# Performance work log

Hardware: AMD Instinct MI355X
Metric: run time of the kernel (lower is better)

Reference implementation:

```python
import jax, jax.numpy as jnp
import numpy as np

B, S, E, H = 4, 2048, 512, 1024

def setup_inputs() -> dict:
    key = jax.random.key(0)
    ks = jax.random.split(key, 8)
    s = 1.0 / np.sqrt(H)
    return {
        "hidden_states": jax.random.normal(ks[0], (B, S, H), jnp.float32),
        "external_embeddings": jax.random.normal(ks[1], (B, E, H), jnp.float32),
        "Wq": jax.random.normal(ks[2], (H, H), jnp.float32) * s,
        "bq": jax.random.normal(ks[3], (H,), jnp.float32) * 0.02,
        "Wk": jax.random.normal(ks[4], (H, H), jnp.float32) * s,
        "bk": jax.random.normal(ks[5], (H,), jnp.float32) * 0.02,
        "Wv": jax.random.normal(ks[6], (H, H), jnp.float32) * s,
        "bv": jax.random.normal(ks[7], (H,), jnp.float32) * 0.02,
    }

def reference(hidden_states, external_embeddings, Wq, bq, Wk, bk, Wv, bv):
    # Projections (torch Linear semantics: here weights stored as [in,out])
    q = hidden_states @ Wq + bq              # [B,S,H]
    k_tok = hidden_states @ Wk + bk          # [B,S,H]
    v_tok = hidden_states @ Wv + bv          # [B,S,H]
    k_ext = external_embeddings @ Wk + bk    # [B,E,H]
    v_ext = external_embeddings @ Wv + bv    # [B,E,H]
    # Each token attends to [its own key] ++ [external keys]; NO 1/sqrt(d) scaling
    # and NO head splitting, matching the original forward exactly.
    s_self = jnp.einsum('bsh,bsh->bs', q, k_tok)[..., None]   # [B,S,1]
    s_ext = jnp.einsum('bsh,beh->bse', q, k_ext)              # [B,S,E]
    scores = jnp.concatenate([s_self, s_ext], axis=-1)        # [B,S,1+E]
    probs = jax.nn.softmax(scores, axis=-1)
    ctx = probs[..., :1] * v_tok + jnp.einsum('bse,beh->bsh', probs[..., 1:], v_ext)
    return ctx  # [B,S,H]
```

## Files before the change

### kernel.cpp

```cpp
#include <hip/hip_runtime.h>
#include <stdint.h>

#define BB 4
#define SS 2048
#define EE 512
#define HH 1024

typedef _Float16 f16;
typedef __attribute__((ext_vector_type(8))) _Float16 f16x8;
typedef __attribute__((ext_vector_type(4))) _Float16 f16x4;
typedef __attribute__((ext_vector_type(4))) float f32x4;

__device__ __forceinline__ void async16(void* lds, const void* g) {
  __builtin_amdgcn_global_load_lds(
      (const __attribute__((address_space(1))) unsigned int*)g,
      (__attribute__((address_space(3))) unsigned int*)lds, 16, 0, 0);
}

#define MFMA16 __builtin_amdgcn_mfma_f32_16x16x32_f16

__global__ __launch_bounds__(256) void prep_kernel(
    const float* __restrict__ xh32, const float* __restrict__ xe32,
    const float* __restrict__ Wq, const float* __restrict__ Wk,
    const float* __restrict__ Wv,
    f16* __restrict__ xh, f16* __restrict__ xe,
    f16* __restrict__ wt_hi, f16* __restrict__ wt_lo) {
  __shared__ float tile[32][33];
  const int bid = blockIdx.x;
  if (bid < 10240) {
    const int i = bid * 256 + threadIdx.x;
    const int n4h = 8192 * HH / 4;
    const float* src = i < n4h ? xh32 : xe32;
    f16* dst = i < n4h ? xh : xe;
    const int k = i < n4h ? i : i - n4h;
    const float4 v = ((const float4*)src)[k];
    f16x4 o;
    o.x = (f16)v.x; o.y = (f16)v.y; o.z = (f16)v.z; o.w = (f16)v.w;
    ((f16x4*)dst)[k] = o;
  } else {
    const int b2 = bid - 10240;
    const int k0 = (b2 & 31) * 32;
    const int n0g = (b2 >> 5) * 32;
    const int which = n0g >> 10;
    const float* W = which == 0 ? Wq : (which == 1 ? Wk : Wv);
    const int n0 = n0g & 1023;
    const int tx = threadIdx.x & 31, ty = threadIdx.x >> 5;
#pragma unroll
    for (int i = 0; i < 32; i += 8)
      tile[ty + i][tx] = W[(size_t)(k0 + ty + i) * 1024 + n0 + tx];
    __syncthreads();
#pragma unroll
    for (int i = 0; i < 32; i += 8) {
      const int np = n0g + ty + i;
      const float v = tile[tx][ty + i];
      const size_t idx = (size_t)np * 1024 + k0 + tx;
      const f16 h = (f16)v;
      wt_hi[idx] = h;
      wt_lo[idx] = (f16)(v - (float)h);
    }
  }
}

__global__ __launch_bounds__(512, 2) void proj_kernel(
    const f16* __restrict__ xh, const f16* __restrict__ xe,
    const f16* __restrict__ wt_hi, const f16* __restrict__ wt_lo,
    const float* __restrict__ bq, const float* __restrict__ bk,
    const float* __restrict__ bv, f16* __restrict__ q_hi, f16* __restrict__ q_lo,
    f16* __restrict__ kt, f16* __restrict__ vt,
    f16* __restrict__ ke_hi, f16* __restrict__ ke_lo, f16* __restrict__ veT) {
  const int g = blockIdx.x;
  const int j = g & 7;
  const int s = g >> 3;
  int mrow0, colB0;
  bool ext = false, splitB = false;
  if (s < 20) {
    splitB = true;
    if (s < 16) {
      colB0 = (s >> 2) * 256;
      mrow0 = ((s & 3) * 8 + j) * 256;
    } else {
      ext = true;
      colB0 = 1024 + (s - 16) * 256;
      mrow0 = j * 256;
    }
  } else {
    const int s2 = s - 20;
    if (s2 < 32) {
      colB0 = (4 + (s2 >> 2)) * 256;
      mrow0 = ((s2 & 3) * 8 + j) * 256;
    } else {
      ext = true;
      colB0 = 1024 + (4 + (s2 - 32)) * 256;
      mrow0 = j * 256;
    }
  }
  const int NT = splitB ? 32 : 16;

  __shared__ f16 lds[65536];

  const int tid = threadIdx.x;
  const int wave = tid >> 6, lane = tid & 63;
  const int wm = wave >> 2, wn = wave & 3;
  const int frow = lane & 15, qd = lane >> 4;

  const f16* A0 = (ext ? xe : xh) + (size_t)mrow0 * HH;
  const f16* Bhi = wt_hi + (size_t)colB0 * HH;
  const f16* Blo = wt_lo + (size_t)colB0 * HH;

  const int srow = tid >> 2;
  const int scol = ((tid & 3) ^ ((srow >> 1) & 3)) * 8;
  const size_t gO0 = (size_t)srow * HH + scol;
  const size_t gO1 = (size_t)(128 + srow) * HH + scol;
  const int ldst0 = (wave * 64) * 8;
  const int ldst1 = (512 + wave * 64) * 8;

  int offA[8], offB[4];
#pragma unroll
  for (int i = 0; i < 8; ++i) {
    const int r = wm * 128 + i * 16 + frow;
    offA[i] = r * 32 + ((qd ^ ((r >> 1) & 3)) * 8);
  }
#pragma unroll
  for (int jj = 0; jj < 4; ++jj) {
    const int r = wn * 64 + jj * 16 + frow;
    offB[jj] = r * 32 + ((qd ^ ((r >> 1) & 3)) * 8);
  }

  f32x4 acc[8][4];
#pragma unroll
  for (int i = 0; i < 8; ++i)
#pragma unroll
    for (int jj = 0; jj < 4; ++jj)
#pragma unroll
      for (int r = 0; r < 4; ++r) acc[i][jj][r] = 0.0f;

  {
    f16* dA0 = &lds[0];
    f16* dB0 = &lds[32768];
    f16* dA1 = &lds[8192];
    f16* dB1 = &lds[32768 + 8192];
    async16(&dA0[ldst0], A0 + gO0);       async16(&dA0[ldst1], A0 + gO1);
    async16(&dB0[ldst0], Bhi + gO0);      async16(&dB0[ldst1], Bhi + gO1);
    async16(&dA1[ldst0], A0 + 32 + gO0);  async16(&dA1[ldst1], A0 + 32 + gO1);
    async16(&dB1[ldst0], Bhi + 32 + gO0); async16(&dB1[ldst1], Bhi + 32 + gO1);
  }
  asm volatile("s_waitcnt vmcnt(4)" ::: "memory");
  __builtin_amdgcn_s_barrier();

  for (int t = 0; t < NT; ++t) {
    const int cur = t & 1, nxt = cur ^ 1;
    const bool st = (t + 1 < NT);
    const int kn = ((t + 1) & 15) * 64;
    const f16* An = A0 + kn;
    const f16* Bn = (((t + 1) & 16) ? Blo : Bhi) + kn;
    const f16* lA0 = &lds[(cur * 2 + 0) * 8192];
    const f16* lB0 = &lds[32768 + (cur * 2 + 0) * 8192];
    const f16* lA1 = &lds[(cur * 2 + 1) * 8192];
    const f16* lB1 = &lds[32768 + (cur * 2 + 1) * 8192];
    f16* sA0 = &lds[(nxt * 2 + 0) * 8192];
    f16* sB0 = &lds[32768 + (nxt * 2 + 0) * 8192];
    f16* sA1 = &lds[(nxt * 2 + 1) * 8192];
    f16* sB1 = &lds[32768 + (nxt * 2 + 1) * 8192];

    f16x8 a[8], b0, b1;

#pragma unroll
    for (int i = 0; i < 8; ++i) a[i] = *(const f16x8*)&lA0[offA[i]];
    b0 = *(const f16x8*)&lB0[offB[0]];
    b1 = *(const f16x8*)&lB0[offB[1]];
    if (st) { async16(&sA0[ldst0], An + gO0); async16(&sA0[ldst1], An + gO1); }
    __builtin_amdgcn_s_barrier();
    __builtin_amdgcn_s_setprio(1);
#pragma unroll
    for (int i = 0; i < 8; ++i) {
      acc[i][0] = MFMA16(a[i], b0, acc[i][0], 0, 0, 0);
      acc[i][1] = MFMA16(a[i], b1, acc[i][1], 0, 0, 0);
    }
    __builtin_amdgcn_s_setprio(0);
    __builtin_amdgcn_s_barrier();

    b0 = *(const f16x8*)&lB0[offB[2]];
    b1 = *(const f16x8*)&lB0[offB[3]];
    if (st) { async16(&sB0[ldst0], Bn + gO0); async16(&sB0[ldst1], Bn + gO1); }
    __builtin_amdgcn_s_barrier();
    __builtin_amdgcn_s_setprio(1);
#pragma unroll
    for (int i = 0; i < 8; ++i) {
      acc[i][2] = MFMA16(a[i], b0, acc[i][2], 0, 0, 0);
      acc[i][3] = MFMA16(a[i], b1, acc[i][3], 0, 0, 0);
    }
    __builtin_amdgcn_s_setprio(0);
    if (t == NT - 1) {
      asm volatile("s_waitcnt vmcnt(0)" ::: "memory");
    } else {
      asm volatile("s_waitcnt vmcnt(4)" ::: "memory");
    }
    __builtin_amdgcn_s_barrier();

#pragma unroll
    for (int i = 0; i < 8; ++i) a[i] = *(const f16x8*)&lA1[offA[i]];
    b0 = *(const f16x8*)&lB1[offB[0]];
    b1 = *(const f16x8*)&lB1[offB[1]];
    if (st) { async16(&sA1[ldst0], An + 32 + gO0); async16(&sA1[ldst1], An + 32 + gO1); }
    __builtin_amdgcn_s_barrier();
    __builtin_amdgcn_s_setprio(1);
#pragma unroll
    for (int i = 0; i < 8; ++i) {
      acc[i][0] = MFMA16(a[i], b0, acc[i][0], 0, 0, 0);
      acc[i][1] = MFMA16(a[i], b1, acc[i][1], 0, 0, 0);
    }
    __builtin_amdgcn_s_setprio(0);
    __builtin_amdgcn_s_barrier();

    b0 = *(const f16x8*)&lB1[offB[2]];
    b1 = *(const f16x8*)&lB1[offB[3]];
    if (st) { async16(&sB1[ldst0], Bn + 32 + gO0); async16(&sB1[ldst1], Bn + 32 + gO1); }
    __builtin_amdgcn_s_barrier();
    __builtin_amdgcn_s_setprio(1);
#pragma unroll
    for (int i = 0; i < 8; ++i) {
      acc[i][2] = MFMA16(a[i], b0, acc[i][2], 0, 0, 0);
      acc[i][3] = MFMA16(a[i], b1, acc[i][3], 0, 0, 0);
    }
    __builtin_amdgcn_s_setprio(0);
    asm volatile("s_waitcnt vmcnt(4)" ::: "memory");
    __builtin_amdgcn_s_barrier();
  }

  const int er0 = wm * 128 + qd * 4;
  const int ec0 = wn * 64 + frow;
  float bias[4];
#pragma unroll
  for (int jj = 0; jj < 4; ++jj) {
    const int c = colB0 + ec0 + jj * 16;
    bias[jj] = c < 1024 ? bq[c] : (c < 2048 ? bk[c - 1024] : bv[c - 2048]);
  }

  if (!ext) {
    if (colB0 < 1024) {
#pragma unroll
      for (int jj = 0; jj < 4; ++jj) {
        const int c = colB0 + ec0 + jj * 16;
#pragma unroll
        for (int i = 0; i < 8; ++i)
#pragma unroll
          for (int r = 0; r < 4; ++r) {
            const int row = mrow0 + er0 + i * 16 + r;
            const float val = acc[i][jj][r] + bias[jj];
            const size_t idx = (size_t)row * HH + c;
            const f16 h = (f16)val;
            q_hi[idx] = h;
            q_lo[idx] = (f16)(val - (float)h);
          }
      }
    } else if (colB0 < 2048) {
#pragma unroll
      for (int jj = 0; jj < 4; ++jj) {
        const int c = colB0 + ec0 + jj * 16 - 1024;
#pragma unroll
        for (int i = 0; i < 8; ++i)
#pragma unroll
          for (int r = 0; r < 4; ++r) {
            const int row = mrow0 + er0 + i * 16 + r;
            kt[(size_t)row * HH + c] = (f16)(acc[i][jj][r] + bias[jj]);
          }
      }
    } else {
#pragma unroll
      for (int jj = 0; jj < 4; ++jj) {
        const int c = colB0 + ec0 + jj * 16 - 2048;
#pragma unroll
        for (int i = 0; i < 8; ++i)
#pragma unroll
          for (int r = 0; r < 4; ++r) {
            const int row = mrow0 + er0 + i * 16 + r;
            vt[(size_t)row * HH + c] = (f16)(acc[i][jj][r] + bias[jj]);
          }
      }
    }
  } else {
    if (colB0 < 2048) {
#pragma unroll
      for (int jj = 0; jj < 4; ++jj) {
        const int c = colB0 + ec0 + jj * 16 - 1024;
#pragma unroll
        for (int i = 0; i < 8; ++i)
#pragma unroll
          for (int r = 0; r < 4; ++r) {
            const int row = mrow0 + er0 + i * 16 + r;
            const float val = acc[i][jj][r] + bias[jj];
            const size_t idx = (size_t)row * HH + c;
            const f16 h = (f16)val;
            ke_hi[idx] = h;
            ke_lo[idx] = (f16)(val - (float)h);
          }
      }
    } else {
      f16* tl = lds;
      const int b = mrow0 >> 9, e0 = mrow0 & 511;
      const int h0 = colB0 - 2048;
#pragma unroll
      for (int p = 0; p < 2; ++p) {
        __syncthreads();
        if ((wn >> 1) == p) {
          const int hL = (wn & 1) * 64 + frow;
#pragma unroll
          for (int jj = 0; jj < 4; ++jj)
#pragma unroll
            for (int i = 0; i < 8; ++i)
#pragma unroll
              for (int r = 0; r < 4; ++r) {
                const int e = er0 + i * 16 + r;
                tl[(hL + jj * 16) * 264 + e] = (f16)(acc[i][jj][r] + bias[jj]);
              }
        }
        __syncthreads();
        for (int c = tid; c < 128 * 32; c += 512) {
          const int hL = c >> 5, ch = c & 31;
          const f16x8 v = *(const f16x8*)&tl[hL * 264 + ch * 8];
          *(f16x8*)&veT[(size_t)(b * HH + h0 + p * 128 + hL) * EE + e0 + ch * 8] = v;
        }
      }
    }
  }
}

__global__ __launch_bounds__(512, 1) void score_kernel(
    const f16* __restrict__ q_hi, const f16* __restrict__ q_lo,
    const f16* __restrict__ ke_hi, const f16* __restrict__ ke_lo,
    float* __restrict__ s_part) {
  const int b = blockIdx.z & 3;
  const int khalf = blockIdx.z >> 2;
  const int mtile = blockIdx.y;
  const int ntile = blockIdx.x;

  __shared__ f16 lds[73728];

  const int tid = threadIdx.x;
  const int wave = tid >> 6, lane = tid & 63;
  const int wm = wave >> 1, wn = wave & 1;
  const int frow = lane & 15, qd = lane >> 4;

  const size_t aoff = ((size_t)b * SS + mtile * 256) * HH + khalf * 512;
  const size_t boff = ((size_t)b * EE + ntile * 128) * HH + khalf * 512;
  const f16* Ah = q_hi + aoff;
  const f16* Al = q_lo + aoff;
  const f16* Bh = ke_hi + boff;
  const f16* Bl = ke_lo + boff;

  const int srow = tid >> 2;
  const int scol = ((tid & 3) ^ ((srow >> 1) & 3)) * 8;
  const size_t gA0 = (size_t)srow * HH + scol;
  const size_t gA1 = (size_t)(128 + srow) * HH + scol;
  const int ldstA0 = (wave * 64) * 8;
  const int ldstA1 = (512 + wave * 64) * 8;
  const int ldstB0 = (wave * 64) * 8;

  int offA[4], offB[4];
#pragma unroll
  for (int i = 0; i < 4; ++i) {
    const int r = wm * 64 + i * 16 + frow;
    offA[i] = r * 32 + ((qd ^ ((r >> 1) & 3)) * 8);
  }
#pragma unroll
  for (int jj = 0; jj < 4; ++jj) {
    const int r = wn * 64 + jj * 16 + frow;
    offB[jj] = r * 32 + ((qd ^ ((r >> 1) & 3)) * 8);
  }

  f32x4 acc[4][4];
#pragma unroll
  for (int i = 0; i < 4; ++i)
#pragma unroll
    for (int jj = 0; jj < 4; ++jj)
#pragma unroll
      for (int r = 0; r < 4; ++r) acc[i][jj][r] = 0.0f;

#pragma unroll
  for (int p = 0; p < 2; ++p) {
    f16* dAh = &lds[p * 24576];
    f16* dAl = &lds[p * 24576 + 8192];
    f16* dBh = &lds[p * 24576 + 16384];
    f16* dBl = &lds[p * 24576 + 20480];
    const int ko = p * 32;
    async16(&dAh[ldstA0], Ah + ko + gA0); async16(&dAh[ldstA1], Ah + ko + gA1);
    async16(&dBh[ldstB0], Bh + ko + gA0);
    async16(&dBl[ldstB0], Bl + ko + gA0);
    async16(&dAl[ldstA0], Al + ko + gA0); async16(&dAl[ldstA1], Al + ko + gA1);
  }
  asm volatile("s_waitcnt vmcnt(6)" ::: "memory");
  __builtin_amdgcn_s_barrier();

  int cur = 0, stg = 2;
  for (int t = 0; t < 16; ++t) {
    const bool st = (t < 14);
    const int kk = (t + 2) * 32;
    const f16* lAh = &lds[cur * 24576];
    const f16* lAl = &lds[cur * 24576 + 8192];
    const f16* lBh = &lds[cur * 24576 + 16384];
    const f16* lBl = &lds[cur * 24576 + 20480];

    if (st) {
      f16* sAh = &lds[stg * 24576];
      f16* sAl = &lds[stg * 24576 + 8192];
      f16* sBh = &lds[stg * 24576 + 16384];
      f16* sBl = &lds[stg * 24576 + 20480];
      async16(&sAh[ldstA0], Ah + kk + gA0); async16(&sAh[ldstA1], Ah + kk + gA1);
      async16(&sBh[ldstB0], Bh + kk + gA0);
      async16(&sBl[ldstB0], Bl + kk + gA0);
      async16(&sAl[ldstA0], Al + kk + gA0); async16(&sAl[ldstA1], Al + kk + gA1);
    }

    f16x8 ah[4], bh[4], bl[4], al[4];
#pragma unroll
    for (int i = 0; i < 4; ++i) ah[i] = *(const f16x8*)&lAh[offA[i]];
#pragma unroll
    for (int jj = 0; jj < 4; ++jj) bh[jj] = *(const f16x8*)&lBh[offB[jj]];
#pragma unroll
    for (int jj = 0; jj < 4; ++jj) bl[jj] = *(const f16x8*)&lBl[offB[jj]];
#pragma unroll
    for (int i = 0; i < 4; ++i) al[i] = *(const f16x8*)&lAl[offA[i]];

    __builtin_amdgcn_s_setprio(1);
#pragma unroll
    for (int i = 0; i < 4; ++i)
#pragma unroll
      for (int jj = 0; jj < 4; ++jj) {
        acc[i][jj] = MFMA16(ah[i], bh[jj], acc[i][jj], 0, 0, 0);
        acc[i][jj] = MFMA16(ah[i], bl[jj], acc[i][jj], 0, 0, 0);
        acc[i][jj] = MFMA16(al[i], bh[jj], acc[i][jj], 0, 0, 0);
      }
    __builtin_amdgcn_s_setprio(0);

    if (st) { asm volatile("s_waitcnt vmcnt(6)" ::: "memory"); }
    else    { asm volatile("s_waitcnt vmcnt(0)" ::: "memory"); }
    __builtin_amdgcn_s_barrier();

    cur = (cur == 2) ? 0 : cur + 1;
    stg = (stg == 2) ? 0 : stg + 1;
  }

  float* dst = s_part + (size_t)khalf * BB * SS * EE + (size_t)b * SS * EE;
#pragma unroll
  for (int jj = 0; jj < 4; ++jj) {
    const int e = ntile * 128 + wn * 64 + jj * 16 + frow;
#pragma unroll
    for (int i = 0; i < 4; ++i)
#pragma unroll
      for (int r = 0; r < 4; ++r) {
        const int s = mtile * 256 + wm * 64 + i * 16 + qd * 4 + r;
        dst[(size_t)s * EE + e] = acc[i][jj][r];
      }
  }
}

__global__ __launch_bounds__(256) void softmax_kernel(
    const f16* __restrict__ q_hi, const f16* __restrict__ q_lo,
    const f16* __restrict__ kt, const float* __restrict__ s_part,
    f16* __restrict__ probs, float* __restrict__ p_self) {
  const int t = blockIdx.x * 4 + (threadIdx.x >> 6);
  const int lane = threadIdx.x & 63;

  const size_t base = (size_t)t * HH;
  float ss = 0.f;
#pragma unroll
  for (int it = 0; it < 4; ++it) {
    const int off = it * 256 + lane * 4;
    const f16x4 qh = *(const f16x4*)&q_hi[base + off];
    const f16x4 ql = *(const f16x4*)&q_lo[base + off];
    const f16x4 kh = *(const f16x4*)&kt[base + off];
    ss += ((float)qh.x + (float)ql.x) * (float)kh.x;
    ss += ((float)qh.y + (float)ql.y) * (float)kh.y;
    ss += ((float)qh.z + (float)ql.z) * (float)kh.z;
    ss += ((float)qh.w + (float)ql.w) * (float)kh.w;
  }
#pragma unroll
  for (int m = 32; m > 0; m >>= 1) ss += __shfl_xor(ss, m, 64);

  const float* r0 = s_part + (size_t)t * EE;
  const float* r1 = s_part + (size_t)BB * SS * EE + (size_t)t * EE;
  const float4 a0 = *(const float4*)&r0[lane * 4];
  const float4 a1 = *(const float4*)&r0[256 + lane * 4];
  const float4 c0 = *(const float4*)&r1[lane * 4];
  const float4 c1 = *(const float4*)&r1[256 + lane * 4];
  const float v0x = a0.x + c0.x, v0y = a0.y + c0.y, v0z = a0.z + c0.z, v0w = a0.w + c0.w;
  const float v1x = a1.x + c1.x, v1y = a1.y + c1.y, v1z = a1.z + c1.z, v1w = a1.w + c1.w;
  float m = fmaxf(fmaxf(fmaxf(v0x, v0y), fmaxf(v0z, v0w)),
                  fmaxf(fmaxf(v1x, v1y), fmaxf(v1z, v1w)));
#pragma unroll
  for (int sh = 32; sh > 0; sh >>= 1) m = fmaxf(m, __shfl_xor(m, sh, 64));
  m = fmaxf(m, ss);
  const float e0 = __expf(v0x - m), e1 = __expf(v0y - m);
  const float e2 = __expf(v0z - m), e3 = __expf(v0w - m);
  const float e4 = __expf(v1x - m), e5 = __expf(v1y - m);
  const float e6 = __expf(v1z - m), e7 = __expf(v1w - m);
  float sum = ((e0 + e1) + (e2 + e3)) + ((e4 + e5) + (e6 + e7));
#pragma unroll
  for (int sh = 32; sh > 0; sh >>= 1) sum += __shfl_xor(sum, sh, 64);
  const float es = __expf(ss - m);
  const float inv = 1.0f / (sum + es);
  f16x4 p0, p1;
  p0.x = (f16)(e0 * inv); p0.y = (f16)(e1 * inv);
  p0.z = (f16)(e2 * inv); p0.w = (f16)(e3 * inv);
  p1.x = (f16)(e4 * inv); p1.y = (f16)(e5 * inv);
  p1.z = (f16)(e6 * inv); p1.w = (f16)(e7 * inv);
  *(f16x4*)&probs[(size_t)t * EE + lane * 4] = p0;
  *(f16x4*)&probs[(size_t)t * EE + 256 + lane * 4] = p1;
  if (lane == 0) p_self[t] = es * inv;
}

__global__ __launch_bounds__(512, 2) void pv_kernel(
    const f16* __restrict__ probs, const f16* __restrict__ veT,
    const float* __restrict__ p_self, const f16* __restrict__ vt,
    float* __restrict__ out) {
  const int b = blockIdx.z;
  const int mtile = blockIdx.y;
  const int ntile = blockIdx.x;

  __shared__ f16 lds[36864];

  const int tid = threadIdx.x;
  const int wave = tid >> 6, lane = tid & 63;
  const int wm = wave >> 1, wn = wave & 1;
  const int frow = lane & 15, qd = lane >> 4;

  const size_t aoff = ((size_t)b * SS + mtile * 256) * EE;
  const size_t boff = ((size_t)b * HH + ntile * 128) * EE;
  const f16* A = probs + aoff;
  const f16* Bv = veT + boff;

  const int srow = tid >> 2;
  const int scol = ((tid & 3) ^ ((srow >> 1) & 3)) * 8;
  const size_t gA0 = (size_t)srow * EE + scol;
  const size_t gA1 = (size_t)(128 + srow) * EE + scol;
  const int ldstA0 = (wave * 64) * 8;
  const int ldstA1 = (512 + wave * 64) * 8;
  const int ldstB0 = (wave * 64) * 8;

  int offA[4], offB[4];
#pragma unroll
  for (int i = 0; i < 4; ++i) {
    const int r = wm * 64 + i * 16 + frow;
    offA[i] = r * 32 + ((qd ^ ((r >> 1) & 3)) * 8);
  }
#pragma unroll
  for (int jj = 0; jj < 4; ++jj) {
    const int r = wn * 64 + jj * 16 + frow;
    offB[jj] = r * 32 + ((qd ^ ((r >> 1) & 3)) * 8);
  }

  f32x4 acc[4][4];
#pragma unroll
  for (int i = 0; i < 4; ++i)
#pragma unroll
    for (int jj = 0; jj < 4; ++jj)
#pragma unroll
      for (int r = 0; r < 4; ++r) acc[i][jj][r] = 0.0f;

  {
    f16* dA0 = &lds[0], *dB0 = &lds[8192];
    f16* dA1 = &lds[12288], *dB1 = &lds[12288 + 8192];
    async16(&dA0[ldstA0], A + gA0); async16(&dA0[ldstA1], A + gA1);
    async16(&dB0[ldstB0], Bv + gA0);
    async16(&dA1[ldstA0], A + 32 + gA0); async16(&dA1[ldstA1], A + 32 + gA1);
    async16(&dB1[ldstB0], Bv + 32 + gA0);
  }
  asm volatile("s_waitcnt vmcnt(3)" ::: "memory");
  __builtin_amdgcn_s_barrier();

  int cur = 0, stg = 2;
  for (int t = 0; t < 16; ++t) {
    const bool st = (t < 14);
    const int kk = (t + 2) * 32;
    const f16* lA = &lds[cur * 12288];
    const f16* lB = &lds[cur * 12288 + 8192];

    if (st) {
      f16* sA = &lds[stg * 12288];
      f16* sB = &lds[stg * 12288 + 8192];
      async16(&sA[ldstA0], A + kk + gA0); async16(&sA[ldstA1], A + kk + gA1);
      async16(&sB[ldstB0], Bv + kk + gA0);
    }

    f16x8 a[4], bb[4];
#pragma unroll
    for (int i = 0; i < 4; ++i) a[i] = *(const f16x8*)&lA[offA[i]];
#pragma unroll
    for (int jj = 0; jj < 4; ++jj) bb[jj] = *(const f16x8*)&lB[offB[jj]];

    __builtin_amdgcn_s_setprio(1);
#pragma unroll
    for (int i = 0; i < 4; ++i)
#pragma unroll
      for (int jj = 0; jj < 4; ++jj)
        acc[i][jj] = MFMA16(a[i], bb[jj], acc[i][jj], 0, 0, 0);
    __builtin_amdgcn_s_setprio(0);

    if (st) { asm volatile("s_waitcnt vmcnt(3)" ::: "memory"); }
    else    { asm volatile("s_waitcnt vmcnt(0)" ::: "memory"); }
    __builtin_amdgcn_s_barrier();

    cur = (cur == 2) ? 0 : cur + 1;
    stg = (stg == 2) ? 0 : stg + 1;
  }

#pragma unroll
  for (int jj = 0; jj < 4; ++jj) {
    const int h = ntile * 128 + wn * 64 + jj * 16 + frow;
#pragma unroll
    for (int i = 0; i < 4; ++i)
#pragma unroll
      for (int r = 0; r < 4; ++r) {
        const int s = mtile * 256 + wm * 64 + i * 16 + qd * 4 + r;
        const size_t t = (size_t)b * SS + s;
        __builtin_nontemporal_store(
            acc[i][jj][r] + p_self[t] * (float)vt[t * HH + h], &out[t * HH + h]);
      }
  }
}

extern "C" void kernel_launch(void* const* d_in, const int* in_sizes, int n_in,
                              void* d_out, int out_size, void* d_ws, size_t ws_size,
                              hipStream_t stream) {
  const float* hidden = (const float*)d_in[0];
  const float* ext    = (const float*)d_in[1];
  const float* Wq = (const float*)d_in[2];
  const float* bq = (const float*)d_in[3];
  const float* Wk = (const float*)d_in[4];
  const float* bk = (const float*)d_in[5];
  const float* Wv = (const float*)d_in[6];
  const float* bv = (const float*)d_in[7];
  float* out = (float*)d_out;

  char* ws = (char*)d_ws;
  size_t off = 0;
  auto alloc = [&](size_t bytes) {
    char* p = ws + off;
    off += (bytes + 255) & ~(size_t)255;
    return p;
  };
  const size_t TOK = 8192, EXT = 2048;
  f16* xh    = (f16*)alloc(TOK * HH * 2);
  f16* xe    = (f16*)alloc(EXT * HH * 2);
  f16* wt_hi = (f16*)alloc(3072ull * HH * 2);
  f16* wt_lo = (f16*)alloc(3072ull * HH * 2);
  f16* q_hi  = (f16*)alloc(TOK * HH * 2);
  f16* q_lo  = (f16*)alloc(TOK * HH * 2);
  f16* kt    = (f16*)alloc(TOK * HH * 2);
  f16* vt    = (f16*)alloc(TOK * HH * 2);
  f16* ke_hi = (f16*)alloc(EXT * HH * 2);
  f16* ke_lo = (f16*)alloc(EXT * HH * 2);
  f16* veT   = (f16*)alloc((size_t)BB * HH * EE * 2);
  float* p_self = (float*)alloc(TOK * 4);
  float* s_part = (float*)alloc(2ull * BB * SS * EE * 4);
  f16* probs    = (f16*)alloc((size_t)BB * SS * EE * 2);

  prep_kernel<<<13312, 256, 0, stream>>>(hidden, ext, Wq, Wk, Wv,
                                         xh, xe, wt_hi, wt_lo);

  proj_kernel<<<448, 512, 0, stream>>>(
      xh, xe, wt_hi, wt_lo, bq, bk, bv,
      q_hi, q_lo, kt, vt, ke_hi, ke_lo, veT);

  score_kernel<<<dim3(4, 8, 8), 512, 0, stream>>>(q_hi, q_lo, ke_hi, ke_lo, s_part);
  softmax_kernel<<<2048, 256, 0, stream>>>(q_hi, q_lo, kt, s_part, probs, p_self);
  pv_kernel<<<dim3(8, 8, 4), 512, 0, stream>>>(probs, veT, p_self, vt, out);
}
```

Measured before the change: 280.6 us.

## Fuse score GEMM, self-score dot and softmax into one attention kernel

Replaces the split-K score kernel and the separate softmax kernel with one kernel. Each block covers 32 query rows across all 512 external keys, so the full score row stays in registers. The self-score dot product is computed from the staged Q/K tiles, and the row softmax is reduced through LDS before fp16 probabilities are written. This removes the fp32 partial-score round trip through global memory and one launch. In exchange, tiles are smaller (32x512 per block), giving less reuse of the external keys. It uses double buffering with a full vmcnt(0) wait every iteration and runs only 256 blocks.

```diff
diff --git a/kernel.cpp b/kernel.cpp
--- a/kernel.cpp
+++ b/kernel.cpp
@@ -9,6 +9,7 @@
 typedef _Float16 f16;
 typedef __attribute__((ext_vector_type(8))) _Float16 f16x8;
 typedef __attribute__((ext_vector_type(4))) _Float16 f16x4;
+typedef __attribute__((ext_vector_type(2))) _Float16 f16x2;
 typedef __attribute__((ext_vector_type(4))) float f32x4;
 
 __device__ __forceinline__ void async16(void* lds, const void* g) {
@@ -325,105 +326,110 @@
   }
 }
 
-__global__ __launch_bounds__(512, 1) void score_kernel(
+__global__ __launch_bounds__(512, 1) void attn_kernel(
     const f16* __restrict__ q_hi, const f16* __restrict__ q_lo,
     const f16* __restrict__ ke_hi, const f16* __restrict__ ke_lo,
-    float* __restrict__ s_part) {
-  const int b = blockIdx.z & 3;
-  const int khalf = blockIdx.z >> 2;
-  const int mtile = blockIdx.y;
-  const int ntile = blockIdx.x;
-
-  __shared__ f16 lds[73728];
+    const f16* __restrict__ kt,
+    f16* __restrict__ probs, float* __restrict__ p_self) {
+  const int mt = blockIdx.x;
+  const int b = blockIdx.y;
+  const int row0 = mt * 32;
+
+  __shared__ f16 lds[72960];
 
   const int tid = threadIdx.x;
   const int wave = tid >> 6, lane = tid & 63;
-  const int wm = wave >> 1, wn = wave & 1;
   const int frow = lane & 15, qd = lane >> 4;
-
-  const size_t aoff = ((size_t)b * SS + mtile * 256) * HH + khalf * 512;
-  const size_t boff = ((size_t)b * EE + ntile * 128) * HH + khalf * 512;
-  const f16* Ah = q_hi + aoff;
-  const f16* Al = q_lo + aoff;
-  const f16* Bh = ke_hi + boff;
-  const f16* Bl = ke_lo + boff;
-
-  const int srow = tid >> 2;
-  const int scol = ((tid & 3) ^ ((srow >> 1) & 3)) * 8;
-  const size_t gA0 = (size_t)srow * HH + scol;
-  const size_t gA1 = (size_t)(128 + srow) * HH + scol;
-  const int ldstA0 = (wave * 64) * 8;
-  const int ldstA1 = (512 + wave * 64) * 8;
-  const int ldstB0 = (wave * 64) * 8;
-
-  int offA[4], offB[4];
-#pragma unroll
-  for (int i = 0; i < 4; ++i) {
-    const int r = wm * 64 + i * 16 + frow;
-    offA[i] = r * 32 + ((qd ^ ((r >> 1) & 3)) * 8);
-  }
+  const int wn = wave;
+
+  const size_t qbase = ((size_t)b * SS + row0) * HH;
+  const f16* Ah = q_hi + qbase;
+  const f16* Al = q_lo + qbase;
+  const f16* Kt = kt + qbase;
+  const size_t kebase = (size_t)b * EE * HH;
+  const f16* Bhg = ke_hi + kebase;
+  const f16* Blg = ke_lo + kebase;
+
+  const int srB = tid >> 2;
+  const int scB = ((tid & 3) ^ ((srB >> 1) & 3)) * 8;
+  const int srA = (tid & 127) >> 2;
+  const int scA = ((tid & 3) ^ ((srA >> 1) & 3)) * 8;
+
+  int offB[4], offA[2];
 #pragma unroll
   for (int jj = 0; jj < 4; ++jj) {
     const int r = wn * 64 + jj * 16 + frow;
     offB[jj] = r * 32 + ((qd ^ ((r >> 1) & 3)) * 8);
   }
-
-  f32x4 acc[4][4];
-#pragma unroll
-  for (int i = 0; i < 4; ++i)
+#pragma unroll
+  for (int i = 0; i < 2; ++i) {
+    const int r = i * 16 + frow;
+    offA[i] = r * 32 + ((qd ^ ((r >> 1) & 3)) * 8);
+  }
+
+  const int sdRow = tid >> 4;
+  const int sdE0 = (tid & 15) * 2;
+  const int sdOff = sdRow * 32 + (((sdE0 >> 3) ^ ((sdRow >> 1) & 3)) * 8) + (sdE0 & 7);
+
+  f32x4 acc[2][4];
+#pragma unroll
+  for (int i = 0; i < 2; ++i)
 #pragma unroll
     for (int jj = 0; jj < 4; ++jj)
 #pragma unroll
       for (int r = 0; r < 4; ++r) acc[i][jj][r] = 0.0f;
-
-#pragma unroll
-  for (int p = 0; p < 2; ++p) {
-    f16* dAh = &lds[p * 24576];
-    f16* dAl = &lds[p * 24576 + 8192];
-    f16* dBh = &lds[p * 24576 + 16384];
-    f16* dBl = &lds[p * 24576 + 20480];
-    const int ko = p * 32;
-    async16(&dAh[ldstA0], Ah + ko + gA0); async16(&dAh[ldstA1], Ah + ko + gA1);
-    async16(&dBh[ldstB0], Bh + ko + gA0);
-    async16(&dBl[ldstB0], Bl + ko + gA0);
-    async16(&dAl[ldstA0], Al + ko + gA0); async16(&dAl[ldstA1], Al + ko + gA1);
-  }
-  asm volatile("s_waitcnt vmcnt(6)" ::: "memory");
+  float ss = 0.f;
+
+  auto STAGE = [&](int p, int ko) {
+    f16* base = &lds[p * 35840];
+#pragma unroll
+    for (int c = 0; c < 4; ++c) {
+      const size_t g = (size_t)(c * 128 + srB) * HH + ko + scB;
+      async16(&base[c * 4096 + wave * 512], Bhg + g);
+    }
+#pragma unroll
+    for (int c = 0; c < 4; ++c) {
+      const size_t g = (size_t)(c * 128 + srB) * HH + ko + scB;
+      async16(&base[16384 + c * 4096 + wave * 512], Blg + g);
+    }
+    if (wave < 6) {
+      const size_t g = (size_t)srA * HH + ko + scA;
+      const f16* src = wave < 2 ? Ah : (wave < 4 ? Al : Kt);
+      const int rbase = 32768 + (wave < 2 ? 0 : (wave < 4 ? 1024 : 2048));
+      async16(&base[rbase + (wave & 1) * 512], src + g);
+    }
+  };
+
+  STAGE(0, 0);
+  asm volatile("s_waitcnt vmcnt(0)" ::: "memory");
   __builtin_amdgcn_s_barrier();
 
-  int cur = 0, stg = 2;
-  for (int t = 0; t < 16; ++t) {
-    const bool st = (t < 14);
-    const int kk = (t + 2) * 32;
-    const f16* lAh = &lds[cur * 24576];
-    const f16* lAl = &lds[cur * 24576 + 8192];
-    const f16* lBh = &lds[cur * 24576 + 16384];
-    const f16* lBl = &lds[cur * 24576 + 20480];
-
-    if (st) {
-      f16* sAh = &lds[stg * 24576];
-      f16* sAl = &lds[stg * 24576 + 8192];
-      f16* sBh = &lds[stg * 24576 + 16384];
-      f16* sBl = &lds[stg * 24576 + 20480];
-      async16(&sAh[ldstA0], Ah + kk + gA0); async16(&sAh[ldstA1], Ah + kk + gA1);
-      async16(&sBh[ldstB0], Bh + kk + gA0);
-      async16(&sBl[ldstB0], Bl + kk + gA0);
-      async16(&sAl[ldstA0], Al + kk + gA0); async16(&sAl[ldstA1], Al + kk + gA1);
-    }
-
-    f16x8 ah[4], bh[4], bl[4], al[4];
-#pragma unroll
-    for (int i = 0; i < 4; ++i) ah[i] = *(const f16x8*)&lAh[offA[i]];
-#pragma unroll
-    for (int jj = 0; jj < 4; ++jj) bh[jj] = *(const f16x8*)&lBh[offB[jj]];
-#pragma unroll
-    for (int jj = 0; jj < 4; ++jj) bl[jj] = *(const f16x8*)&lBl[offB[jj]];
-#pragma unroll
-    for (int i = 0; i < 4; ++i) al[i] = *(const f16x8*)&lAl[offA[i]];
+  for (int t = 0; t < 32; ++t) {
+    const int cur = t & 1;
+    if (t < 31) STAGE(cur ^ 1, (t + 1) * 32);
+
+    const f16* base = &lds[cur * 35840];
+    f16x8 bh[4], bl[4], ah[2], al[2];
+#pragma unroll
+    for (int jj = 0; jj < 4; ++jj) bh[jj] = *(const f16x8*)&base[offB[jj]];
+#pragma unroll
+    for (int jj = 0; jj < 4; ++jj) bl[jj] = *(const f16x8*)&base[16384 + offB[jj]];
+#pragma unroll
+    for (int i = 0; i < 2; ++i) ah[i] = *(const f16x8*)&base[32768 + offA[i]];
+#pragma unroll
+    for (int i = 0; i < 2; ++i) al[i] = *(const f16x8*)&base[33792 + offA[i]];
+
+    {
+      const f16x2 a2 = *(const f16x2*)&base[32768 + sdOff];
+      const f16x2 l2 = *(const f16x2*)&base[33792 + sdOff];
+      const f16x2 k2 = *(const f16x2*)&base[34816 + sdOff];
+      ss += ((float)a2.x + (float)l2.x) * (float)k2.x;
+      ss += ((float)a2.y + (float)l2.y) * (float)k2.y;
+    }
 
     __builtin_amdgcn_s_setprio(1);
 #pragma unroll
-    for (int i = 0; i < 4; ++i)
+    for (int i = 0; i < 2; ++i)
 #pragma unroll
       for (int jj = 0; jj < 4; ++jj) {
         acc[i][jj] = MFMA16(ah[i], bh[jj], acc[i][jj], 0, 0, 0);
@@ -432,81 +438,96 @@
       }
     __builtin_amdgcn_s_setprio(0);
 
-    if (st) { asm volatile("s_waitcnt vmcnt(6)" ::: "memory"); }
-    else    { asm volatile("s_waitcnt vmcnt(0)" ::: "memory"); }
-    __builtin_amdgcn_s_barrier();
-
-    cur = (cur == 2) ? 0 : cur + 1;
-    stg = (stg == 2) ? 0 : stg + 1;
-  }
-
-  float* dst = s_part + (size_t)khalf * BB * SS * EE + (size_t)b * SS * EE;
-#pragma unroll
-  for (int jj = 0; jj < 4; ++jj) {
-    const int e = ntile * 128 + wn * 64 + jj * 16 + frow;
-#pragma unroll
-    for (int i = 0; i < 4; ++i)
-#pragma unroll
-      for (int r = 0; r < 4; ++r) {
-        const int s = mtile * 256 + wm * 64 + i * 16 + qd * 4 + r;
-        dst[(size_t)s * EE + e] = acc[i][jj][r];
-      }
-  }
-}
-
-__global__ __launch_bounds__(256) void softmax_kernel(
-    const f16* __restrict__ q_hi, const f16* __restrict__ q_lo,
-    const f16* __restrict__ kt, const float* __restrict__ s_part,
-    f16* __restrict__ probs, float* __restrict__ p_self) {
-  const int t = blockIdx.x * 4 + (threadIdx.x >> 6);
-  const int lane = threadIdx.x & 63;
-
-  const size_t base = (size_t)t * HH;
-  float ss = 0.f;
-#pragma unroll
-  for (int it = 0; it < 4; ++it) {
-    const int off = it * 256 + lane * 4;
-    const f16x4 qh = *(const f16x4*)&q_hi[base + off];
-    const f16x4 ql = *(const f16x4*)&q_lo[base + off];
-    const f16x4 kh = *(const f16x4*)&kt[base + off];
-    ss += ((float)qh.x + (float)ql.x) * (float)kh.x;
-    ss += ((float)qh.y + (float)ql.y) * (float)kh.y;
-    ss += ((float)qh.z + (float)ql.z) * (float)kh.z;
-    ss += ((float)qh.w + (float)ql.w) * (float)kh.w;
-  }
-#pragma unroll
-  for (int m = 32; m > 0; m >>= 1) ss += __shfl_xor(ss, m, 64);
-
-  const float* r0 = s_part + (size_t)t * EE;
-  const float* r1 = s_part + (size_t)BB * SS * EE + (size_t)t * EE;
-  const float4 a0 = *(const float4*)&r0[lane * 4];
-  const float4 a1 = *(const float4*)&r0[256 + lane * 4];
-  const float4 c0 = *(const float4*)&r1[lane * 4];
-  const float4 c1 = *(const float4*)&r1[256 + lane * 4];
-  const float v0x = a0.x + c0.x, v0y = a0.y + c0.y, v0z = a0.z + c0.z, v0w = a0.w + c0.w;
-  const float v1x = a1.x + c1.x, v1y = a1.y + c1.y, v1z = a1.z + c1.z, v1w = a1.w + c1.w;
-  float m = fmaxf(fmaxf(fmaxf(v0x, v0y), fmaxf(v0z, v0w)),
-                  fmaxf(fmaxf(v1x, v1y), fmaxf(v1z, v1w)));
-#pragma unroll
-  for (int sh = 32; sh > 0; sh >>= 1) m = fmaxf(m, __shfl_xor(m, sh, 64));
-  m = fmaxf(m, ss);
-  const float e0 = __expf(v0x - m), e1 = __expf(v0y - m);
-  const float e2 = __expf(v0z - m), e3 = __expf(v0w - m);
-  const float e4 = __expf(v1x - m), e5 = __expf(v1y - m);
-  const float e6 = __expf(v1z - m), e7 = __expf(v1w - m);
-  float sum = ((e0 + e1) + (e2 + e3)) + ((e4 + e5) + (e6 + e7));
-#pragma unroll
-  for (int sh = 32; sh > 0; sh >>= 1) sum += __shfl_xor(sum, sh, 64);
-  const float es = __expf(ss - m);
-  const float inv = 1.0f / (sum + es);
-  f16x4 p0, p1;
-  p0.x = (f16)(e0 * inv); p0.y = (f16)(e1 * inv);
-  p0.z = (f16)(e2 * inv); p0.w = (f16)(e3 * inv);
-  p1.x = (f16)(e4 * inv); p1.y = (f16)(e5 * inv);
-  p1.z = (f16)(e6 * inv); p1.w = (f16)(e7 * inv);
-  *(f16x4*)&probs[(size_t)t * EE + lane * 4] = p0;
-  *(f16x4*)&probs[(size_t)t * EE + 256 + lane * 4] = p1;
-  if (lane == 0) p_self[t] = es * inv;
+    asm volatile("s_waitcnt vmcnt(0)" ::: "memory");
+    __builtin_amdgcn_s_barrier();
+  }
+
+  float* ssrow = (float*)&lds[71680];
+  float* wmax = ssrow + 32;
+  float* wsum = wmax + 256;
+  float* gmax = wsum + 256;
+  float* ginv = gmax + 32;
+
+#pragma unroll
+  for (int m2 = 1; m2 < 16; m2 <<= 1) ss += __shfl_xor(ss, m2, 16);
+  if ((tid & 15) == 0) ssrow[sdRow] = ss;
+
+  float pm[2][4];
+#pragma unroll
+  for (int i = 0; i < 2; ++i)
+#pragma unroll
+    for (int r = 0; r < 4; ++r) {
+      float m = fmaxf(fmaxf(acc[i][0][r], acc[i][1][r]),
+                      fmaxf(acc[i][2][r], acc[i][3][r]));
+#pragma unroll
+      for (int s2 = 1; s2 < 16; s2 <<= 1) m = fmaxf(m, __shfl_xor(m, s2, 16));
+      pm[i][r] = m;
+    }
+  if (frow == 0) {
+#pragma unroll
+    for (int i = 0; i < 2; ++i)
+#pragma unroll
+      for (int r = 0; r < 4; ++r)
+        wmax[(i * 16 + qd * 4 + r) * 8 + wn] = pm[i][r];
+  }
+  __syncthreads();
+
+  if (tid < 32) {
+    float m = wmax[tid * 8];
+#pragma unroll
+    for (int w = 1; w < 8; ++w) m = fmaxf(m, wmax[tid * 8 + w]);
+    gmax[tid] = fmaxf(m, ssrow[tid]);
+  }
+  __syncthreads();
+
+  float psum[2][4];
+#pragma unroll
+  for (int i = 0; i < 2; ++i)
+#pragma unroll
+    for (int r = 0; r < 4; ++r) {
+      const float gm = gmax[i * 16 + qd * 4 + r];
+      float s = 0.f;
+#pragma unroll
+      for (int jj = 0; jj < 4; ++jj) {
+        const float e = __expf(acc[i][jj][r] - gm);
+        acc[i][jj][r] = e;
+        s += e;
+      }
+#pragma unroll
+      for (int s2 = 1; s2 < 16; s2 <<= 1) s += __shfl_xor(s, s2, 16);
+      psum[i][r] = s;
+    }
+  if (frow == 0) {
+#pragma unroll
+    for (int i = 0; i < 2; ++i)
+#pragma unroll
+      for (int r = 0; r < 4; ++r)
+        wsum[(i * 16 + qd * 4 + r) * 8 + wn] = psum[i][r];
+  }
+  __syncthreads();
+
+  if (tid < 32) {
+    float s = 0.f;
+#pragma unroll
+    for (int w = 0; w < 8; ++w) s += wsum[tid * 8 + w];
+    const float es = __expf(ssrow[tid] - gmax[tid]);
+    const float inv = 1.0f / (s + es);
+    ginv[tid] = inv;
+    p_self[(size_t)b * SS + row0 + tid] = es * inv;
+  }
+  __syncthreads();
+
+#pragma unroll
+  for (int i = 0; i < 2; ++i)
+#pragma unroll
+    for (int r = 0; r < 4; ++r) {
+      const int row = i * 16 + qd * 4 + r;
+      const float inv = ginv[row];
+      const size_t rb = ((size_t)b * SS + row0 + row) * EE;
+#pragma unroll
+      for (int jj = 0; jj < 4; ++jj)
+        probs[rb + wn * 64 + jj * 16 + frow] = (f16)(acc[i][jj][r] * inv);
+    }
 }
 
 __global__ __launch_bounds__(512, 2) void pv_kernel(
@@ -652,7 +673,6 @@
   f16* ke_lo = (f16*)alloc(EXT * HH * 2);
   f16* veT   = (f16*)alloc((size_t)BB * HH * EE * 2);
   float* p_self = (float*)alloc(TOK * 4);
-  float* s_part = (float*)alloc(2ull * BB * SS * EE * 4);
   f16* probs    = (f16*)alloc((size_t)BB * SS * EE * 2);
 
   prep_kernel<<<13312, 256, 0, stream>>>(hidden, ext, Wq, Wk, Wv,
@@ -662,7 +682,7 @@
       xh, xe, wt_hi, wt_lo, bq, bk, bv,
       q_hi, q_lo, kt, vt, ke_hi, ke_lo, veT);
 
-  score_kernel<<<dim3(4, 8, 8), 512, 0, stream>>>(q_hi, q_lo, ke_hi, ke_lo, s_part);
-  softmax_kernel<<<2048, 256, 0, stream>>>(q_hi, q_lo, kt, s_part, probs, p_self);
+  attn_kernel<<<dim3(64, 4), 512, 0, stream>>>(q_hi, q_lo, ke_hi, ke_lo, kt,
+                                               probs, p_self);
   pv_kernel<<<dim3(8, 8, 4), 512, 0, stream>>>(probs, veT, p_self, vt, out);
 }
```

Result: slower. 331.9 us (+18.3%).
